# Kernel tuning notes

Measured on AMD Instinct MI355X. Metric: run time of the kernel, lower is better.

Reference implementation:

```python
import jax, jax.numpy as jnp
import numpy as np

LN_EPS = 1e-5

def _layer_norm(x):
    m = jnp.mean(x, axis=-1, keepdims=True)
    v = jnp.mean(jnp.square(x - m), axis=-1, keepdims=True)
    return (x - m) / jnp.sqrt(v + LN_EPS)

def setup_inputs() -> dict:
    key = jax.random.key(0)
    ks = jax.random.split(key, 6)
    B, S, d_in, d_out = 8, 2048, 1024, 4096
    x = jax.random.normal(ks[0], (B, S, d_in), dtype=jnp.float32)
    # torch.randn % 1 -> values in [0, 1)
    weight_in = jax.random.uniform(ks[1], (d_out, d_in), dtype=jnp.float32)
    bias_in = jax.random.uniform(ks[2], (d_out,), dtype=jnp.float32)
    weight_out = jax.random.uniform(ks[3], (d_in, d_out), dtype=jnp.float32)
    bias_out = jax.random.uniform(ks[4], (d_in,), dtype=jnp.float32)
    lengths = jax.random.randint(ks[5], (B,), 1, S + 1, dtype=jnp.int64 if jax.config.read('jax_enable_x64') else jnp.int32)
    return {"x": x, "weight_in": weight_in, "bias_in": bias_in,
            "weight_out": weight_out, "bias_out": bias_out, "lengths": lengths}

def reference(x, weight_in, bias_in, weight_out, bias_out, lengths):
    # lengths is unused mathematically in the dense baseline (ragged kernels
    # only skip padded rows; valid-region math identical).
    for _ in range(10):
        x = jnp.einsum('bsd,od->bso', x, weight_in) + bias_in  # [B,S,d_out]
        x = _layer_norm(x)
        x = jnp.einsum('bso,do->bsd', x, weight_out) + bias_out  # [B,S,d_in]
        x = _layer_norm(x)
    return x
```

## Files before the change

kernel.cpp:

```cpp
#include <hip/hip_runtime.h>


typedef __attribute__((ext_vector_type(4))) float    f32x4;
typedef __attribute__((ext_vector_type(8))) _Float16 f16x8;
typedef __attribute__((ext_vector_type(4))) _Float16 f16x4;

#define LN_EPS 1e-5f

__device__ __forceinline__ ushort f2h_bits(float f) {
    union { _Float16 h; ushort u; } c; c.h = (_Float16)f; return c.u;
}

typedef const __attribute__((address_space(1))) void* gas_ptr;
typedef __attribute__((address_space(3))) void* las_ptr;

__device__ __forceinline__ void gload_lds16(const void* g, void* l) {
    __builtin_amdgcn_global_load_lds((gas_ptr)g, (las_ptr)l, 16, 0, 0);
}

__device__ __forceinline__ f16x8 ldf(const _Float16* base, int byteoff) {
    return *reinterpret_cast<const f16x8*>(
        reinterpret_cast<const char*>(base) + byteoff);
}

__global__ __launch_bounds__(256) void conv_f32_f16(
        const float* __restrict__ in, _Float16* __restrict__ outp, int n4) {
    int i = blockIdx.x * 256 + threadIdx.x;
    if (i >= n4) return;
    float4 f = reinterpret_cast<const float4*>(in)[i];
    f16x4 r;
    r[0] = (_Float16)f.x; r[1] = (_Float16)f.y;
    r[2] = (_Float16)f.z; r[3] = (_Float16)f.w;
    *reinterpret_cast<f16x4*>(&outp[(size_t)i * 4]) = r;
}

template<int W>
__global__ __launch_bounds__(256)
void rowsum_rows(const _Float16* __restrict__ w, float* __restrict__ outp) {
    const int wid  = threadIdx.x >> 6;
    const int lane = threadIdx.x & 63;
    const size_t row = (size_t)blockIdx.x * 4 + wid;
    const _Float16* p = w + row * W;
    float s = 0.f;
    #pragma unroll
    for (int i = 0; i < W / 512; ++i) {
        f16x8 v = *reinterpret_cast<const f16x8*>(p + i * 512 + lane * 8);
        #pragma unroll
        for (int j = 0; j < 8; ++j) s += (float)v[j];
    }
    #pragma unroll
    for (int off = 32; off > 0; off >>= 1) s += __shfl_xor(s, off);
    if (lane == 0) outp[row] = s;
}

__global__ __launch_bounds__(256) void init_ident_stats(float2* __restrict__ st) {
    int i = blockIdx.x * 256 + threadIdx.x;
    st[i] = make_float2(0.f, 1.f);
}

template<int NP, int W>
__global__ __launch_bounds__(256)
void reduce_stats(const float2* __restrict__ part, float2* __restrict__ st) {
    const int wid  = threadIdx.x >> 6;
    const int lane = threadIdx.x & 63;
    const size_t row = (size_t)blockIdx.x * 4 + wid;
    float s = 0.f, q = 0.f;
    if (lane < NP) {
        float2 p = part[row * NP + lane];
        s = p.x; q = p.y;
    }
    #pragma unroll
    for (int off = 32; off > 0; off >>= 1) {
        s += __shfl_xor(s, off);
        q += __shfl_xor(q, off);
    }
    if (lane == 0) {
        const float mean = s * (1.0f / W);
        const float var  = fmaxf(q * (1.0f / W) - mean * mean, 0.f);
        st[row] = make_float2(mean, rsqrtf(var + LN_EPS));
    }
}

template<int M, int N, int K, int PANELS>
__global__ __launch_bounds__(512)
void gemm256_ln(const _Float16* __restrict__ A, const _Float16* __restrict__ B,
                const float* __restrict__ bias, const float* __restrict__ wsum,
                const float2* __restrict__ stats, _Float16* __restrict__ C,
                float2* __restrict__ partials) {
    constexpr int NT     = K / 64;
    constexpr int NIT    = NT / 2;
    constexpr int NBX    = N / 256;
    constexpr int NTILES = PANELS * NT;
    constexpr int NWG    = (M / (256 * PANELS)) * NBX;

    __shared__ __attribute__((aligned(16))) _Float16 lds[2][2][2][8192];

    const int tid  = threadIdx.x;
    const int wid  = tid >> 6;
    const int lane = tid & 63;
    const int wr   = wid >> 2;
    const int wc   = wid & 3;

    int bn0, bm0b;
    if constexpr (NBX == 16) {
        const int x = blockIdx.x & 7, j = blockIdx.x >> 3;
        bn0  = (x * 2 + (j & 1)) * 256;
        bm0b = (j >> 1) * (256 * PANELS);
    } else {
        int bid = (blockIdx.x & 7) * (NWG >> 3) + (blockIdx.x >> 3);
        bn0  = (bid % NBX) * 256;
        bm0b = (bid / NBX) * (256 * PANELS);
    }

    const int trow = tid >> 3;
    const int cg   = (tid & 7) ^ (trow & 7);
    const _Float16* Bsrc = B + (size_t)(bn0 + trow) * K + cg * 8;

    const int fr  = lane & 15;
    const int fq  = lane >> 4;
    const int s8  = lane & 7;
    const int cb0 = ((fq       ^ s8) << 4);
    const int cb1 = (((4 + fq) ^ s8) << 4);
    const int brb = (wc & 1) * 64;

    const _Float16* Ah[2] = { &lds[0][0][wr][0],      &lds[1][0][wr][0] };
    const _Float16* Bh[2] = { &lds[0][1][wc >> 1][0], &lds[1][1][wc >> 1][0] };

#define STAGE_A(buf, h, t) do { \
    const int _tt = (t) & (NTILES - 1); \
    const _Float16* _as = A + (size_t)(bm0b + (_tt / NT) * 256 + (h) * 128 + trow) * K \
                            + (_tt % NT) * 64 + cg * 8; \
    gload_lds16(_as,                  (void*)&lds[buf][0][h][       wid*512]); \
    gload_lds16(_as + (size_t)64 * K, (void*)&lds[buf][0][h][4096 + wid*512]); } while(0)
#define STAGE_B(buf, h, t) do { \
    const int _kk = ((t) & (NT - 1)) * 64; \
    gload_lds16(Bsrc + (size_t)((h)*128     ) * K + _kk, (void*)&lds[buf][1][h][       wid*512]); \
    gload_lds16(Bsrc + (size_t)((h)*128 + 64) * K + _kk, (void*)&lds[buf][1][h][4096 + wid*512]); } while(0)

#define READ_ALO(b) do { _Pragma("unroll") for (int i = 0; i < 4; ++i) { \
    aLo[i][0] = ldf(Ah[b], (i*16+fr)*128 + cb0); \
    aLo[i][1] = ldf(Ah[b], (i*16+fr)*128 + cb1); } } while(0)
#define READ_AHI(b) do { _Pragma("unroll") for (int i = 0; i < 4; ++i) { \
    aHi[i][0] = ldf(Ah[b], ((i+4)*16+fr)*128 + cb0); \
    aHi[i][1] = ldf(Ah[b], ((i+4)*16+fr)*128 + cb1); } } while(0)
#define READ_BLO(b) do { _Pragma("unroll") for (int j = 0; j < 2; ++j) { \
    bLo[j][0] = ldf(Bh[b], (brb + j*16 + fr)*128 + cb0); \
    bLo[j][1] = ldf(Bh[b], (brb + j*16 + fr)*128 + cb1); } } while(0)
#define READ_BHI(b) do { _Pragma("unroll") for (int j = 0; j < 2; ++j) { \
    bHi[j][0] = ldf(Bh[b], (brb + (j+2)*16 + fr)*128 + cb0); \
    bHi[j][1] = ldf(Bh[b], (brb + (j+2)*16 + fr)*128 + cb1); } } while(0)

#define MFMA_BLK(AF, ioff, BF, joff) do { \
    _Pragma("unroll") for (int i = 0; i < 4; ++i) \
    _Pragma("unroll") for (int j = 0; j < 2; ++j) { \
        acc[i+ioff][j+joff] = __builtin_amdgcn_mfma_f32_16x16x32_f16(AF[i][0], BF[j][0], acc[i+ioff][j+joff], 0, 0, 0); \
        acc[i+ioff][j+joff] = __builtin_amdgcn_mfma_f32_16x16x32_f16(AF[i][1], BF[j][1], acc[i+ioff][j+joff], 0, 0, 0); } } while(0)

#define BARRIER() __builtin_amdgcn_s_barrier()
#define VMCNT4()  asm volatile("s_waitcnt vmcnt(4)" ::: "memory")

    STAGE_B(0, 0, 0); STAGE_B(0, 1, 0);
    STAGE_A(0, 0, 0); STAGE_A(0, 1, 0);
    STAGE_B(1, 0, 1); STAGE_B(1, 1, 1);
    VMCNT4();
    BARRIER();

    float bcol[4], wcol[4];
    #pragma unroll
    for (int j = 0; j < 4; ++j) {
        const int c = bn0 + wc * 64 + j * 16 + fr;
        bcol[j] = bias[c]; wcol[j] = wsum[c];
    }

    for (int p = 0; p < PANELS; ++p) {
        f32x4 acc[8][4] = {};
        f16x8 aLo[4][2], aHi[4][2], bLo[2][2], bHi[2][2];

        for (int it = 0; it < NIT; ++it) {
            const int T = p * NT + 2 * it;
            READ_ALO(0); READ_BLO(0);
            STAGE_A(1, 0, T + 1);
            BARRIER();
            __builtin_amdgcn_s_setprio(1); MFMA_BLK(aLo, 0, bLo, 0); __builtin_amdgcn_s_setprio(0);
            BARRIER();
            READ_BHI(0);
            STAGE_A(1, 1, T + 1);
            BARRIER();
            __builtin_amdgcn_s_setprio(1); MFMA_BLK(aLo, 0, bHi, 2); __builtin_amdgcn_s_setprio(0);
            BARRIER();
            READ_AHI(0);
            STAGE_B(0, 0, T + 2);
            BARRIER();
            __builtin_amdgcn_s_setprio(1); MFMA_BLK(aHi, 4, bLo, 0); __builtin_amdgcn_s_setprio(0);
            BARRIER();
            STAGE_B(0, 1, T + 2);
            BARRIER();
            __builtin_amdgcn_s_setprio(1); MFMA_BLK(aHi, 4, bHi, 2); __builtin_amdgcn_s_setprio(0);
            VMCNT4();
            BARRIER();
            READ_ALO(1); READ_BLO(1);
            STAGE_A(0, 0, T + 2);
            BARRIER();
            __builtin_amdgcn_s_setprio(1); MFMA_BLK(aLo, 0, bLo, 0); __builtin_amdgcn_s_setprio(0);
            BARRIER();
            READ_BHI(1);
            STAGE_A(0, 1, T + 2);
            BARRIER();
            __builtin_amdgcn_s_setprio(1); MFMA_BLK(aLo, 0, bHi, 2); __builtin_amdgcn_s_setprio(0);
            BARRIER();
            READ_AHI(1);
            STAGE_B(1, 0, T + 3);
            BARRIER();
            __builtin_amdgcn_s_setprio(1); MFMA_BLK(aHi, 4, bLo, 0); __builtin_amdgcn_s_setprio(0);
            BARRIER();
            STAGE_B(1, 1, T + 3);
            BARRIER();
            __builtin_amdgcn_s_setprio(1); MFMA_BLK(aHi, 4, bHi, 2); __builtin_amdgcn_s_setprio(0);
            VMCNT4();
            BARRIER();
        }

        const int bm0 = bm0b + p * 256;
        ushort* eps = (ushort*)&lds[1][0][0][0];
        #pragma unroll
        for (int pass = 0; pass < 4; ++pass) {
            if (wr == (pass >> 1)) {
                #pragma unroll
                for (int i2 = 0; i2 < 4; ++i2) {
                    const int i = (pass & 1) * 4 + i2;
                    #pragma unroll
                    for (int q = 0; q < 4; ++q) {
                        const int rloc = wr * 128 + i * 16 + fq * 4 + q;
                        const int rl   = rloc - pass * 64;
                        const float2 st = stats[bm0 + rloc];
                        const float rs = st.y, coef = st.y * st.x;
                        const int key = ((rl >> 2) & 3) << 4;
                        #pragma unroll
                        for (int j = 0; j < 4; ++j) {
                            const float v = rs * acc[i][j][q] - coef * wcol[j] + bcol[j];
                            const int c = wc * 64 + j * 16 + fr;
                            eps[rl * 256 + (c ^ key)] = f2h_bits(v);
                        }
                    }
                }
            }
            BARRIER();
            {
                const int rl  = tid >> 3;
                const int a8  = tid & 7;
                const int r   = bm0 + pass * 64 + rl;
                const int key = ((rl >> 2) & 3) << 4;
                float s = 0.f, sq = 0.f;
                ushort* crow = (ushort*)(C + (size_t)r * N + bn0);
                #pragma unroll
                for (int k = 0; k < 4; ++k) {
                    const int ch = 8 * k + a8;
                    uint4 d = *reinterpret_cast<const uint4*>(&eps[rl * 256 + ch * 8]);
                    f16x8 v = *reinterpret_cast<const f16x8*>(&d);
                    #pragma unroll
                    for (int e = 0; e < 8; ++e) {
                        const float f = (float)v[e];
                        s += f; sq += f * f;
                    }
                    *reinterpret_cast<uint4*>(&crow[(ch * 8) ^ key]) = d;
                }
                s  += __shfl_xor(s, 1);  sq += __shfl_xor(sq, 1);
                s  += __shfl_xor(s, 2);  sq += __shfl_xor(sq, 2);
                s  += __shfl_xor(s, 4);  sq += __shfl_xor(sq, 4);
                if (a8 == 0)
                    partials[(size_t)r * NBX + (bn0 >> 8)] = make_float2(s, sq);
            }
            BARRIER();
        }
    }
#undef STAGE_A
#undef STAGE_B
#undef READ_ALO
#undef READ_AHI
#undef READ_BLO
#undef READ_BHI
#undef MFMA_BLK
#undef BARRIER
#undef VMCNT4
}

__global__ __launch_bounds__(256)
void ln_final(const _Float16* __restrict__ a, const float2* __restrict__ st,
              float* __restrict__ outp) {
    const int wid  = threadIdx.x >> 6;
    const int lane = threadIdx.x & 63;
    const size_t row = (size_t)blockIdx.x * 4 + wid;
    const float2 s = st[row];
    const float mean = s.x, rstd = s.y;
    const _Float16* p = a + row * 1024;
    #pragma unroll
    for (int i = 0; i < 2; ++i) {
        f16x8 v = *reinterpret_cast<const f16x8*>(p + i * 512 + lane * 8);
        float* op = outp + row * 1024 + i * 512 + lane * 8;
        float4 o0, o1;
        o0.x = ((float)v[0] - mean) * rstd;
        o0.y = ((float)v[1] - mean) * rstd;
        o0.z = ((float)v[2] - mean) * rstd;
        o0.w = ((float)v[3] - mean) * rstd;
        o1.x = ((float)v[4] - mean) * rstd;
        o1.y = ((float)v[5] - mean) * rstd;
        o1.z = ((float)v[6] - mean) * rstd;
        o1.w = ((float)v[7] - mean) * rstd;
        reinterpret_cast<float4*>(op)[0] = o0;
        reinterpret_cast<float4*>(op)[1] = o1;
    }
}

extern "C" void kernel_launch(void* const* d_in, const int* in_sizes, int n_in,
                              void* d_out, int out_size, void* d_ws, size_t ws_size,
                              hipStream_t stream) {
    const float* x     = (const float*)d_in[0];
    const float* w_in  = (const float*)d_in[1];
    const float* b_in  = (const float*)d_in[2];
    const float* w_out = (const float*)d_in[3];
    const float* b_out = (const float*)d_in[4];

    constexpr int Mrows = 16384;
    constexpr int Din   = 1024;
    constexpr int Dout  = 4096;

    char* ws = (char*)d_ws;
    _Float16* wib = (_Float16*)ws; ws += (size_t)Dout * Din * 2;
    _Float16* wob = (_Float16*)ws; ws += (size_t)Din * Dout * 2;
    _Float16* a2b = (_Float16*)ws; ws += (size_t)Mrows * Din * 2;
    _Float16* a1b = (_Float16*)ws; ws += (size_t)Mrows * Dout * 2;
    float* winsum  = (float*)ws;   ws += Dout * 4;
    float* woutsum = (float*)ws;   ws += Din * 4;
    float2* st1 = (float2*)ws;     ws += (size_t)Mrows * 8;
    float2* st2 = (float2*)ws;     ws += (size_t)Mrows * 8;
    float2* p1  = (float2*)ws;     ws += (size_t)Mrows * 16 * 8;
    float2* p2  = (float2*)ws;

    const dim3 blk(256);

    conv_f32_f16<<<(Dout * Din / 4) / 256, blk, 0, stream>>>(w_in,  wib, Dout * Din / 4);
    conv_f32_f16<<<(Din * Dout / 4) / 256, blk, 0, stream>>>(w_out, wob, Din * Dout / 4);
    conv_f32_f16<<<(Mrows * Din / 4) / 256, blk, 0, stream>>>(x, a2b, Mrows * Din / 4);
    rowsum_rows<Din> <<<Dout / 4, blk, 0, stream>>>(wib, winsum);
    rowsum_rows<Dout><<<Din / 4,  blk, 0, stream>>>(wob, woutsum);
    init_ident_stats<<<Mrows / 128, blk, 0, stream>>>(st2);

    for (int it = 0; it < 10; ++it) {
        gemm256_ln<Mrows, Dout, Din, 1>
            <<<(Mrows / 256) * (Dout / 256), dim3(512), 0, stream>>>(
                a2b, wib, b_in, winsum, st2, a1b, p1);
        reduce_stats<16, Dout><<<Mrows / 4, blk, 0, stream>>>(p1, st1);
        gemm256_ln<Mrows, Din, Dout, 1>
            <<<(Mrows / 256) * (Din / 256), dim3(512), 0, stream>>>(
                a1b, wob, b_out, woutsum, st1, a2b, p2);
        reduce_stats<4, Din><<<Mrows / 4, blk, 0, stream>>>(p2, st2);
    }
    ln_final<<<Mrows / 4, blk, 0, stream>>>(a2b, st2, (float*)d_out);
}
```

Measured before the change: 2.822 ms.

## Fuse row-stat reduction into GEMM via last-block atomic counter

Removes the separate reduce_stats kernels. Each GEMM workgroup now bumps a per-row-panel atomic counter, and the last block to finish a panel reduces the partial sums into mean/rstd. This saves two launches per iteration and a pass over the partials. It also stops prefetching past the last K tile, drops the unused PANELS path, and uses nontemporal stores for the large intermediate activation in the first GEMM. The cost is a serialized tail reduction in one block per panel, plus threadfence and atomic overhead.

Result: slower. 3.946 ms (+39.8%).

```diff
diff --git a/kernel.cpp b/kernel.cpp
--- a/kernel.cpp
+++ b/kernel.cpp
@@ -4,6 +4,7 @@
 typedef __attribute__((ext_vector_type(4))) float    f32x4;
 typedef __attribute__((ext_vector_type(8))) _Float16 f16x8;
 typedef __attribute__((ext_vector_type(4))) _Float16 f16x4;
+typedef __attribute__((ext_vector_type(4))) uint     u32x4;
 
 #define LN_EPS 1e-5f
 
@@ -58,40 +59,22 @@
     st[i] = make_float2(0.f, 1.f);
 }
 
-template<int NP, int W>
-__global__ __launch_bounds__(256)
-void reduce_stats(const float2* __restrict__ part, float2* __restrict__ st) {
-    const int wid  = threadIdx.x >> 6;
-    const int lane = threadIdx.x & 63;
-    const size_t row = (size_t)blockIdx.x * 4 + wid;
-    float s = 0.f, q = 0.f;
-    if (lane < NP) {
-        float2 p = part[row * NP + lane];
-        s = p.x; q = p.y;
-    }
-    #pragma unroll
-    for (int off = 32; off > 0; off >>= 1) {
-        s += __shfl_xor(s, off);
-        q += __shfl_xor(q, off);
-    }
-    if (lane == 0) {
-        const float mean = s * (1.0f / W);
-        const float var  = fmaxf(q * (1.0f / W) - mean * mean, 0.f);
-        st[row] = make_float2(mean, rsqrtf(var + LN_EPS));
-    }
-}
-
-template<int M, int N, int K, int PANELS>
+__global__ __launch_bounds__(256) void zero_u32(unsigned* __restrict__ p, int n) {
+    int i = blockIdx.x * 256 + threadIdx.x;
+    if (i < n) p[i] = 0u;
+}
+
+template<int M, int N, int K, bool NTC>
 __global__ __launch_bounds__(512)
 void gemm256_ln(const _Float16* __restrict__ A, const _Float16* __restrict__ B,
                 const float* __restrict__ bias, const float* __restrict__ wsum,
                 const float2* __restrict__ stats, _Float16* __restrict__ C,
-                float2* __restrict__ partials) {
-    constexpr int NT     = K / 64;
-    constexpr int NIT    = NT / 2;
-    constexpr int NBX    = N / 256;
-    constexpr int NTILES = PANELS * NT;
-    constexpr int NWG    = (M / (256 * PANELS)) * NBX;
+                float2* __restrict__ partials, float2* __restrict__ stats_out,
+                unsigned* __restrict__ ctr) {
+    constexpr int NT  = K / 64;
+    constexpr int NIT = NT / 2;
+    constexpr int NBX = N / 256;
+    constexpr int NWG = (M / 256) * NBX;
 
     __shared__ __attribute__((aligned(16))) _Float16 lds[2][2][2][8192];
 
@@ -101,19 +84,20 @@
     const int wr   = wid >> 2;
     const int wc   = wid & 3;
 
-    int bn0, bm0b;
+    int bn0, bm0;
     if constexpr (NBX == 16) {
         const int x = blockIdx.x & 7, j = blockIdx.x >> 3;
-        bn0  = (x * 2 + (j & 1)) * 256;
-        bm0b = (j >> 1) * (256 * PANELS);
+        bn0 = (x * 2 + (j & 1)) * 256;
+        bm0 = (j >> 1) * 256;
     } else {
         int bid = (blockIdx.x & 7) * (NWG >> 3) + (blockIdx.x >> 3);
-        bn0  = (bid % NBX) * 256;
-        bm0b = (bid / NBX) * (256 * PANELS);
+        bn0 = (bid % NBX) * 256;
+        bm0 = (bid / NBX) * 256;
     }
 
     const int trow = tid >> 3;
     const int cg   = (tid & 7) ^ (trow & 7);
+    const _Float16* Asrc = A + (size_t)(bm0 + trow) * K + cg * 8;
     const _Float16* Bsrc = B + (size_t)(bn0 + trow) * K + cg * 8;
 
     const int fr  = lane & 15;
@@ -126,16 +110,15 @@
     const _Float16* Ah[2] = { &lds[0][0][wr][0],      &lds[1][0][wr][0] };
     const _Float16* Bh[2] = { &lds[0][1][wc >> 1][0], &lds[1][1][wc >> 1][0] };
 
-#define STAGE_A(buf, h, t) do { \
-    const int _tt = (t) & (NTILES - 1); \
-    const _Float16* _as = A + (size_t)(bm0b + (_tt / NT) * 256 + (h) * 128 + trow) * K \
-                            + (_tt % NT) * 64 + cg * 8; \
-    gload_lds16(_as,                  (void*)&lds[buf][0][h][       wid*512]); \
-    gload_lds16(_as + (size_t)64 * K, (void*)&lds[buf][0][h][4096 + wid*512]); } while(0)
-#define STAGE_B(buf, h, t) do { \
-    const int _kk = ((t) & (NT - 1)) * 64; \
-    gload_lds16(Bsrc + (size_t)((h)*128     ) * K + _kk, (void*)&lds[buf][1][h][       wid*512]); \
-    gload_lds16(Bsrc + (size_t)((h)*128 + 64) * K + _kk, (void*)&lds[buf][1][h][4096 + wid*512]); } while(0)
+    f32x4 acc[8][4] = {};
+    f16x8 aLo[4][2], aHi[4][2], bLo[2][2], bHi[2][2];
+
+#define STAGE_A(buf, h, kk) do { \
+    gload_lds16(Asrc + (size_t)((h)*128     ) * K + (kk), (void*)&lds[buf][0][h][       wid*512]); \
+    gload_lds16(Asrc + (size_t)((h)*128 + 64) * K + (kk), (void*)&lds[buf][0][h][4096 + wid*512]); } while(0)
+#define STAGE_B(buf, h, kk) do { \
+    gload_lds16(Bsrc + (size_t)((h)*128     ) * K + (kk), (void*)&lds[buf][1][h][       wid*512]); \
+    gload_lds16(Bsrc + (size_t)((h)*128 + 64) * K + (kk), (void*)&lds[buf][1][h][4096 + wid*512]); } while(0)
 
 #define READ_ALO(b) do { _Pragma("unroll") for (int i = 0; i < 4; ++i) { \
     aLo[i][0] = ldf(Ah[b], (i*16+fr)*128 + cb0); \
@@ -158,10 +141,11 @@
 
 #define BARRIER() __builtin_amdgcn_s_barrier()
 #define VMCNT4()  asm volatile("s_waitcnt vmcnt(4)" ::: "memory")
-
-    STAGE_B(0, 0, 0); STAGE_B(0, 1, 0);
-    STAGE_A(0, 0, 0); STAGE_A(0, 1, 0);
-    STAGE_B(1, 0, 1); STAGE_B(1, 1, 1);
+#define VMCNT0()  asm volatile("s_waitcnt vmcnt(0)" ::: "memory")
+
+    STAGE_B(0, 0, 0);  STAGE_B(0, 1, 0);
+    STAGE_A(0, 0, 0);  STAGE_A(0, 1, 0);
+    STAGE_B(1, 0, 64); STAGE_B(1, 1, 64);
     VMCNT4();
     BARRIER();
 
@@ -172,105 +156,127 @@
         bcol[j] = bias[c]; wcol[j] = wsum[c];
     }
 
-    for (int p = 0; p < PANELS; ++p) {
-        f32x4 acc[8][4] = {};
-        f16x8 aLo[4][2], aHi[4][2], bLo[2][2], bHi[2][2];
-
-        for (int it = 0; it < NIT; ++it) {
-            const int T = p * NT + 2 * it;
-            READ_ALO(0); READ_BLO(0);
-            STAGE_A(1, 0, T + 1);
-            BARRIER();
-            __builtin_amdgcn_s_setprio(1); MFMA_BLK(aLo, 0, bLo, 0); __builtin_amdgcn_s_setprio(0);
-            BARRIER();
-            READ_BHI(0);
-            STAGE_A(1, 1, T + 1);
-            BARRIER();
-            __builtin_amdgcn_s_setprio(1); MFMA_BLK(aLo, 0, bHi, 2); __builtin_amdgcn_s_setprio(0);
-            BARRIER();
-            READ_AHI(0);
-            STAGE_B(0, 0, T + 2);
-            BARRIER();
-            __builtin_amdgcn_s_setprio(1); MFMA_BLK(aHi, 4, bLo, 0); __builtin_amdgcn_s_setprio(0);
-            BARRIER();
-            STAGE_B(0, 1, T + 2);
-            BARRIER();
-            __builtin_amdgcn_s_setprio(1); MFMA_BLK(aHi, 4, bHi, 2); __builtin_amdgcn_s_setprio(0);
-            VMCNT4();
-            BARRIER();
-            READ_ALO(1); READ_BLO(1);
-            STAGE_A(0, 0, T + 2);
-            BARRIER();
-            __builtin_amdgcn_s_setprio(1); MFMA_BLK(aLo, 0, bLo, 0); __builtin_amdgcn_s_setprio(0);
-            BARRIER();
-            READ_BHI(1);
-            STAGE_A(0, 1, T + 2);
-            BARRIER();
-            __builtin_amdgcn_s_setprio(1); MFMA_BLK(aLo, 0, bHi, 2); __builtin_amdgcn_s_setprio(0);
-            BARRIER();
-            READ_AHI(1);
-            STAGE_B(1, 0, T + 3);
-            BARRIER();
-            __builtin_amdgcn_s_setprio(1); MFMA_BLK(aHi, 4, bLo, 0); __builtin_amdgcn_s_setprio(0);
-            BARRIER();
-            STAGE_B(1, 1, T + 3);
-            BARRIER();
-            __builtin_amdgcn_s_setprio(1); MFMA_BLK(aHi, 4, bHi, 2); __builtin_amdgcn_s_setprio(0);
-            VMCNT4();
-            BARRIER();
-        }
-
-        const int bm0 = bm0b + p * 256;
-        ushort* eps = (ushort*)&lds[1][0][0][0];
-        #pragma unroll
-        for (int pass = 0; pass < 4; ++pass) {
-            if (wr == (pass >> 1)) {
+    for (int it = 0; it < NIT; ++it) {
+        const int k1 = it * 128 + 64;
+        const int k2 = it * 128 + 128;
+        const int k3 = it * 128 + 192;
+        const bool pf = (it < NIT - 1);
+
+        READ_ALO(0); READ_BLO(0);
+        STAGE_A(1, 0, k1);
+        BARRIER();
+        __builtin_amdgcn_s_setprio(1); MFMA_BLK(aLo, 0, bLo, 0); __builtin_amdgcn_s_setprio(0);
+        BARRIER();
+        READ_BHI(0);
+        STAGE_A(1, 1, k1);
+        BARRIER();
+        __builtin_amdgcn_s_setprio(1); MFMA_BLK(aLo, 0, bHi, 2); __builtin_amdgcn_s_setprio(0);
+        BARRIER();
+        READ_AHI(0);
+        if (pf) STAGE_B(0, 0, k2);
+        BARRIER();
+        __builtin_amdgcn_s_setprio(1); MFMA_BLK(aHi, 4, bLo, 0); __builtin_amdgcn_s_setprio(0);
+        BARRIER();
+        if (pf) STAGE_B(0, 1, k2);
+        BARRIER();
+        __builtin_amdgcn_s_setprio(1); MFMA_BLK(aHi, 4, bHi, 2); __builtin_amdgcn_s_setprio(0);
+        if (pf) VMCNT4(); else VMCNT0();
+        BARRIER();
+        READ_ALO(1); READ_BLO(1);
+        if (pf) STAGE_A(0, 0, k2);
+        BARRIER();
+        __builtin_amdgcn_s_setprio(1); MFMA_BLK(aLo, 0, bLo, 0); __builtin_amdgcn_s_setprio(0);
+        BARRIER();
+        READ_BHI(1);
+        if (pf) STAGE_A(0, 1, k2);
+        BARRIER();
+        __builtin_amdgcn_s_setprio(1); MFMA_BLK(aLo, 0, bHi, 2); __builtin_amdgcn_s_setprio(0);
+        BARRIER();
+        READ_AHI(1);
+        if (pf) STAGE_B(1, 0, k3);
+        BARRIER();
+        __builtin_amdgcn_s_setprio(1); MFMA_BLK(aHi, 4, bLo, 0); __builtin_amdgcn_s_setprio(0);
+        BARRIER();
+        if (pf) STAGE_B(1, 1, k3);
+        BARRIER();
+        __builtin_amdgcn_s_setprio(1); MFMA_BLK(aHi, 4, bHi, 2); __builtin_amdgcn_s_setprio(0);
+        VMCNT4();
+        BARRIER();
+    }
+
+    ushort* eps = (ushort*)&lds[1][0][0][0];
+    #pragma unroll
+    for (int pass = 0; pass < 4; ++pass) {
+        if (wr == (pass >> 1)) {
+            #pragma unroll
+            for (int i2 = 0; i2 < 4; ++i2) {
+                const int i = (pass & 1) * 4 + i2;
                 #pragma unroll
-                for (int i2 = 0; i2 < 4; ++i2) {
-                    const int i = (pass & 1) * 4 + i2;
+                for (int q = 0; q < 4; ++q) {
+                    const int rloc = wr * 128 + i * 16 + fq * 4 + q;
+                    const int rl   = rloc - pass * 64;
+                    const float2 st = stats[bm0 + rloc];
+                    const float rs = st.y, coef = st.y * st.x;
+                    const int key = ((rl >> 2) & 3) << 4;
                     #pragma unroll
-                    for (int q = 0; q < 4; ++q) {
-                        const int rloc = wr * 128 + i * 16 + fq * 4 + q;
-                        const int rl   = rloc - pass * 64;
-                        const float2 st = stats[bm0 + rloc];
-                        const float rs = st.y, coef = st.y * st.x;
-                        const int key = ((rl >> 2) & 3) << 4;
-                        #pragma unroll
-                        for (int j = 0; j < 4; ++j) {
-                            const float v = rs * acc[i][j][q] - coef * wcol[j] + bcol[j];
-                            const int c = wc * 64 + j * 16 + fr;
-                            eps[rl * 256 + (c ^ key)] = f2h_bits(v);
-                        }
+                    for (int j = 0; j < 4; ++j) {
+                        const float v = rs * acc[i][j][q] - coef * wcol[j] + bcol[j];
+                        const int c = wc * 64 + j * 16 + fr;
+                        eps[rl * 256 + (c ^ key)] = f2h_bits(v);
                     }
                 }
             }
-            BARRIER();
-            {
-                const int rl  = tid >> 3;
-                const int a8  = tid & 7;
-                const int r   = bm0 + pass * 64 + rl;
-                const int key = ((rl >> 2) & 3) << 4;
-                float s = 0.f, sq = 0.f;
-                ushort* crow = (ushort*)(C + (size_t)r * N + bn0);
+        }
+        BARRIER();
+        {
+            const int rl  = tid >> 3;
+            const int a8  = tid & 7;
+            const int r   = bm0 + pass * 64 + rl;
+            const int key = ((rl >> 2) & 3) << 4;
+            float s = 0.f, sq = 0.f;
+            ushort* crow = (ushort*)(C + (size_t)r * N + bn0);
+            #pragma unroll
+            for (int k = 0; k < 4; ++k) {
+                const int ch = 8 * k + a8;
+                u32x4 d = *reinterpret_cast<const u32x4*>(&eps[rl * 256 + ch * 8]);
+                const f16x8 v = *reinterpret_cast<const f16x8*>(&d);
                 #pragma unroll
-                for (int k = 0; k < 4; ++k) {
-                    const int ch = 8 * k + a8;
-                    uint4 d = *reinterpret_cast<const uint4*>(&eps[rl * 256 + ch * 8]);
-                    f16x8 v = *reinterpret_cast<const f16x8*>(&d);
-                    #pragma unroll
-                    for (int e = 0; e < 8; ++e) {
-                        const float f = (float)v[e];
-                        s += f; sq += f * f;
-                    }
-                    *reinterpret_cast<uint4*>(&crow[(ch * 8) ^ key]) = d;
+                for (int e = 0; e < 8; ++e) {
+                    const float f = (float)v[e];
+                    s += f; sq += f * f;
                 }
-                s  += __shfl_xor(s, 1);  sq += __shfl_xor(sq, 1);
-                s  += __shfl_xor(s, 2);  sq += __shfl_xor(sq, 2);
-                s  += __shfl_xor(s, 4);  sq += __shfl_xor(sq, 4);
-                if (a8 == 0)
-                    partials[(size_t)r * NBX + (bn0 >> 8)] = make_float2(s, sq);
+                if constexpr (NTC)
+                    __builtin_nontemporal_store(d, reinterpret_cast<u32x4*>(&crow[(ch * 8) ^ key]));
+                else
+                    *reinterpret_cast<u32x4*>(&crow[(ch * 8) ^ key]) = d;
             }
-            BARRIER();
+            s  += __shfl_xor(s, 1);  sq += __shfl_xor(sq, 1);
+            s  += __shfl_xor(s, 2);  sq += __shfl_xor(sq, 2);
+            s  += __shfl_xor(s, 4);  sq += __shfl_xor(sq, 4);
+            if (a8 == 0)
+                partials[(size_t)r * NBX + (bn0 >> 8)] = make_float2(s, sq);
+        }
+        BARRIER();
+    }
+
+    __syncthreads();
+    int* flag = (int*)&lds[1][0][0][0];
+    if (tid == 0) {
+        __threadfence();
+        unsigned prev = atomicAdd(&ctr[bm0 >> 8], 1u);
+        *flag = (prev == (unsigned)(NBX - 1)) ? 1 : 0;
+    }
+    __syncthreads();
+    if (*flag) {
+        __threadfence();
+        if (tid < 256) {
+            const float2* pr = partials + (size_t)(bm0 + tid) * NBX;
+            float s = 0.f, q = 0.f;
+            #pragma unroll
+            for (int k = 0; k < NBX; ++k) { const float2 v = pr[k]; s += v.x; q += v.y; }
+            const float mean = s * (1.0f / N);
+            const float var  = fmaxf(q * (1.0f / N) - mean * mean, 0.f);
+            stats_out[bm0 + tid] = make_float2(mean, rsqrtf(var + LN_EPS));
         }
     }
 #undef STAGE_A
@@ -282,6 +288,7 @@
 #undef MFMA_BLK
 #undef BARRIER
 #undef VMCNT4
+#undef VMCNT0
 }
 
 __global__ __launch_bounds__(256)
@@ -334,7 +341,8 @@
     float2* st1 = (float2*)ws;     ws += (size_t)Mrows * 8;
     float2* st2 = (float2*)ws;     ws += (size_t)Mrows * 8;
     float2* p1  = (float2*)ws;     ws += (size_t)Mrows * 16 * 8;
-    float2* p2  = (float2*)ws;
+    float2* p2  = (float2*)ws;     ws += (size_t)Mrows * 4 * 8;
+    unsigned* ctrs = (unsigned*)ws;
 
     const dim3 blk(256);
 
@@ -344,16 +352,15 @@
     rowsum_rows<Din> <<<Dout / 4, blk, 0, stream>>>(wib, winsum);
     rowsum_rows<Dout><<<Din / 4,  blk, 0, stream>>>(wob, woutsum);
     init_ident_stats<<<Mrows / 128, blk, 0, stream>>>(st2);
+    zero_u32<<<5, blk, 0, stream>>>(ctrs, 1280);
 
     for (int it = 0; it < 10; ++it) {
-        gemm256_ln<Mrows, Dout, Din, 1>
+        gemm256_ln<Mrows, Dout, Din, true>
             <<<(Mrows / 256) * (Dout / 256), dim3(512), 0, stream>>>(
-                a2b, wib, b_in, winsum, st2, a1b, p1);
-        reduce_stats<16, Dout><<<Mrows / 4, blk, 0, stream>>>(p1, st1);
-        gemm256_ln<Mrows, Din, Dout, 1>
+                a2b, wib, b_in, winsum, st2, a1b, p1, st1, ctrs + it * 64);
+        gemm256_ln<Mrows, Din, Dout, false>
             <<<(Mrows / 256) * (Din / 256), dim3(512), 0, stream>>>(
-                a1b, wob, b_out, woutsum, st1, a2b, p2);
-        reduce_stats<4, Din><<<Mrows / 4, blk, 0, stream>>>(p2, st2);
+                a1b, wob, b_out, woutsum, st1, a2b, p2, st2, ctrs + 640 + it * 64);
     }
     ln_final<<<Mrows / 4, blk, 0, stream>>>(a2b, st2, (float*)d_out);
 }
```
